# Kernel optimization log

Hardware: AMD Instinct MI355X
Metric: run time of the kernel (lower is better)

The kernel has to match this reference:

```python
import jax, jax.numpy as jnp
import numpy as np

SKIP = 2
EPS = 1e-9
K_PEN = 0.01
MU_BG = 0.0
VAR_BG = 100.0
SIZ = (256, 256, 256)
SIZA = (160, 192, 160)
NC = 10
COMPS = np.array([2, 2, 1, 1, 2, 1, 1, 2, 1])
NG = int(COMPS.sum())  # 13
FSIZ = (13, 13, 13)  # round(256*1.0/20)


def setup_inputs() -> dict:
    key = jax.random.key(0)
    ks = jax.random.split(key, 10)
    I = jax.random.uniform(ks[0], SIZ, jnp.float32)
    A = jax.random.uniform(ks[1], (*SIZA, NC), jnp.float32)
    A = A / jnp.sum(A, axis=-1, keepdims=True)  # probabilistic atlas
    aff_I = jnp.eye(4, dtype=jnp.float32)
    aff_A = jnp.diag(jnp.array([SIZ[0] / SIZA[0], SIZ[1] / SIZA[1], SIZ[2] / SIZA[2], 1.0], jnp.float32))
    mus = jax.random.uniform(ks[2], (NG,), jnp.float32)
    vars_ = 0.05 + 0.1 * jax.random.uniform(ks[3], (NG,), jnp.float32)
    w = np.asarray(jax.random.uniform(ks[4], (NG,))) + 0.1
    cls = np.repeat(np.arange(len(COMPS)), COMPS)
    onehot = (cls[:, None] == np.arange(len(COMPS))[None, :]).astype(np.float32)
    w = w / (onehot @ (onehot.T @ w))  # weights sum to 1 within each class
    weights = jnp.asarray(w, jnp.float32)
    gmm_onehot = jnp.asarray(onehot)
    ts = 0.5 * jax.random.normal(ks[5], (3,), jnp.float32)
    thetas = 2.0 * jax.random.normal(ks[6], (3,), jnp.float32)  # degrees
    scalings = 0.5 * jax.random.normal(ks[7], (3,), jnp.float32)
    shears = 0.5 * jax.random.normal(ks[8], (3,), jnp.float32)
    FIELD = 0.5 * jax.random.normal(ks[9], (*FSIZ, 3), jnp.float32)
    return dict(I=I, A=A, aff_I=aff_I, aff_A=aff_A, mus=mus, vars_=vars_, weights=weights,
                gmm_onehot=gmm_onehot, ts=ts, thetas=thetas, scalings=scalings,
                shears=shears, FIELD=FIELD)


def _bspline3(t):
    t = jnp.abs(t)
    return jnp.where(t < 1, (4.0 - 6.0 * t * t + 3.0 * t * t * t) / 6.0,
                     jnp.where(t < 2, (2.0 - t) ** 3 / 6.0, 0.0))


def _cubic_matrix(coords, n):
    # dense [m, n] cubic-B-spline sampling matrix with circular (dft) boundary,
    # prefilter=False (FIELD values treated as spline coefficients)
    m = coords.shape[0]
    base = jnp.floor(coords).astype(jnp.int32)
    W = jnp.zeros((m, n), coords.dtype)
    rows = jnp.arange(m)
    for k in (-1, 0, 1, 2):
        node = base + k
        W = W.at[rows, node % n].add(_bspline3(coords - node))
    return W


def reference(I, A, aff_I, aff_A, mus, vars_, weights, gmm_onehot, ts, thetas, scalings, shears, FIELD):
    nxA, nyA, nzA, C = A.shape
    fx, fy, fz = FIELD.shape[:3]
    dt = I.dtype

    # ---- affine from parameters (T @ Sh @ Sc @ Rz @ Ry @ Rx) ----
    th = thetas * (jnp.pi / 180.0)
    sh = shears / 100.0
    sc = jnp.exp(scalings / 20.0)
    c, s = jnp.cos(th), jnp.sin(th)
    Rx = jnp.array([[1.0, 0.0, 0.0, 0.0], [0.0, c[0], -s[0], 0.0], [0.0, s[0], c[0], 0.0], [0.0, 0.0, 0.0, 1.0]])
    Ry = jnp.array([[c[1], 0.0, s[1], 0.0], [0.0, 1.0, 0.0, 0.0], [-s[1], 0.0, c[1], 0.0], [0.0, 0.0, 0.0, 1.0]])
    Rz = jnp.array([[c[2], -s[2], 0.0, 0.0], [s[2], c[2], 0.0, 0.0], [0.0, 0.0, 1.0, 0.0], [0.0, 0.0, 0.0, 1.0]])
    Sc = jnp.diag(jnp.concatenate([sc, jnp.ones((1,), sc.dtype)]))
    Sh = jnp.array([[1.0, sh[1], sh[2], 0.0], [sh[0], 1.0, sh[2], 0.0], [sh[0], sh[1], 1.0, 0.0], [0.0, 0.0, 0.0, 1.0]])
    T = jnp.eye(4, dtype=dt).at[:3, 3].set(ts)
    AFF = T @ Sh @ Sc @ Rz @ Ry @ Rx
    V = jnp.linalg.inv(AFF @ aff_A) @ aff_I  # image voxel -> atlas voxel

    # ---- cubic-spline resample of deformation field (separable grid) ----
    xs = jnp.arange(0, I.shape[0], SKIP).astype(dt)
    ys = jnp.arange(0, I.shape[1], SKIP).astype(dt)
    zs = jnp.arange(0, I.shape[2], SKIP).astype(dt)
    field_f = FIELD / 100.0 * jnp.array([nxA, nyA, nzA], dt)  # [fx,fy,fz,3]
    Wx = _cubic_matrix(fx * xs / I.shape[0], fx)
    Wy = _cubic_matrix(fy * ys / I.shape[1], fy)
    Wz = _cubic_matrix(fz * zs / I.shape[2], fz)
    t1 = jnp.einsum('ia,abcd->ibcd', Wx, field_f)
    t1 = jnp.einsum('jb,ibcd->ijcd', Wy, t1)
    field_rs = jnp.einsum('kc,ijcd->ijkd', Wz, t1)  # [X,Y,Z,3]

    X = xs[:, None, None]
    Y = ys[None, :, None]
    Z = zs[None, None, :]
    gx = V[0, 0] * X + V[0, 1] * Y + V[0, 2] * Z + V[0, 3] + field_rs[..., 0]
    gy = V[1, 0] * X + V[1, 1] * Y + V[1, 2] * Z + V[1, 3] + field_rs[..., 1]
    gz = V[2, 0] * X + V[2, 1] * Y + V[2, 2] * Z + V[2, 3] + field_rs[..., 2]

    # ---- trilinear pull of atlas (zero bound, no extrapolation) ----
    x0 = jnp.floor(gx).astype(jnp.int32); rx = gx - x0
    y0 = jnp.floor(gy).astype(jnp.int32); ry = gy - y0
    z0 = jnp.floor(gz).astype(jnp.int32); rz = gz - z0
    Af = A.reshape(-1, C)
    acc = jnp.zeros((*gx.shape, C), dt)
    for dx in (0, 1):
        ix = x0 + dx; wx = rx if dx else 1.0 - rx
        vx = (ix >= 0) & (ix < nxA); ixc = jnp.clip(ix, 0, nxA - 1)
        for dy in (0, 1):
            iy = y0 + dy; wy = ry if dy else 1.0 - ry
            vy = (iy >= 0) & (iy < nyA); iyc = jnp.clip(iy, 0, nyA - 1)
            for dz in (0, 1):
                iz = z0 + dz; wz = rz if dz else 1.0 - rz
                vz = (iz >= 0) & (iz < nzA); izc = jnp.clip(iz, 0, nzA - 1)
                w = jnp.where(vx & vy & vz, wx * wy * wz, 0.0)
                flat = (ixc * nyA + iyc) * nzA + izc
                vals = jnp.take(Af, flat.reshape(-1), axis=0).reshape(*flat.shape, C)
                acc = acc + w[..., None] * vals

    atlas_rs = jnp.clip(acc, 0.0, 1.0)
    missing = 1.0 - jnp.sum(atlas_rs, axis=-1)
    prior_bg = jnp.clip(atlas_rs[..., 0] + missing, 0.0, 1.0)
    priors_rest = atlas_rs[..., 1:]  # already clipped to [0,1]
    priors = jnp.concatenate([prior_bg[..., None], priors_rest], axis=-1)

    # ---- GMM likelihoods ----
    Iskip = I[::SKIP, ::SKIP, ::SKIP]
    gl_bg = jnp.exp(-0.5 * (Iskip - MU_BG) ** 2 / VAR_BG) / jnp.sqrt(2.0 * jnp.pi * VAR_BG)
    gl = jnp.exp(-0.5 * (Iskip[..., None] - mus) ** 2 / vars_) / jnp.sqrt(2.0 * jnp.pi * vars_)  # [X,Y,Z,NG]
    class_lh = jnp.einsum('xyzg,gc->xyzc', weights * gl, gmm_onehot)  # per-class mixture
    normalizer = prior_bg * gl_bg + jnp.sum(priors_rest * class_lh, axis=-1)
    log_lh = jnp.log(EPS + normalizer)

    # ---- gradient penalty on field in voxel units of the full image grid ----
    siz_vec = jnp.array(I.shape, dt)
    fsiz_vec = jnp.array(FIELD.shape[:3], dt)
    fv = field_f * (fsiz_vec / siz_vec)
    pen = (jnp.mean((fv[1:] - fv[:-1]) ** 2)
           + jnp.mean((fv[:, 1:] - fv[:, :-1]) ** 2)
           + jnp.mean((fv[:, :, 1:] - fv[:, :, :-1]) ** 2)) / 3.0
    def_pen = K_PEN * pen
    loss = -jnp.mean(log_lh) + def_pen
    grids_new = jnp.stack([gx, gy, gz], axis=-1)
    return (loss, grids_new, priors, def_pen)
```

## Files before the change

kernel.cpp:

```cpp
#include <hip/hip_runtime.h>

#define PI_D 3.14159265358979323846
#define NS 128
#define NVOX (NS*NS*NS)
#define NBLK (NVOX/256)

typedef float f4v __attribute__((ext_vector_type(4)));
typedef f4v f4u __attribute__((aligned(8)));


static __device__ __forceinline__ float bspline3f(float t) {
    t = fabsf(t);
    if (t < 1.0f) return (4.0f - 6.0f*t*t + 3.0f*t*t*t) * (1.0f/6.0f);
    if (t < 2.0f) { float u = 2.0f - t; return u*u*u * (1.0f/6.0f); }
    return 0.0f;
}

static __device__ void mm4(const double* Am, const double* Bm, double* Cm) {
    for (int i = 0; i < 4; i++)
        for (int j = 0; j < 4; j++) {
            double s = 0.0;
            for (int k = 0; k < 4; k++) s += Am[i*4+k] * Bm[k*4+j];
            Cm[i*4+j] = s;
        }
}

static __device__ void inv4(const double* Am, double* Om) {
    double a[4][8];
    for (int i = 0; i < 4; i++)
        for (int j = 0; j < 4; j++) {
            a[i][j]   = Am[i*4+j];
            a[i][4+j] = (i == j) ? 1.0 : 0.0;
        }
    for (int col = 0; col < 4; col++) {
        int piv = col; double best = fabs(a[col][col]);
        for (int r = col+1; r < 4; r++) {
            double v = fabs(a[r][col]);
            if (v > best) { best = v; piv = r; }
        }
        if (piv != col)
            for (int j = 0; j < 8; j++) { double t = a[col][j]; a[col][j] = a[piv][j]; a[piv][j] = t; }
        double d = a[col][col];
        for (int j = 0; j < 8; j++) a[col][j] /= d;
        for (int r = 0; r < 4; r++) if (r != col) {
            double f = a[r][col];
            for (int j = 0; j < 8; j++) a[r][j] -= f * a[col][j];
        }
    }
    for (int i = 0; i < 4; i++)
        for (int j = 0; j < 4; j++) Om[i*4+j] = a[i][4+j];
}


__global__ void AD_prep(const float* __restrict__ aff_I, const float* __restrict__ aff_A,
                        const float* __restrict__ ts, const float* __restrict__ thetas,
                        const float* __restrict__ scalings, const float* __restrict__ shears,
                        const float* __restrict__ FIELD,
                        const float* __restrict__ vars_, const float* __restrict__ weights,
                        const float* __restrict__ mus,
                        float* __restrict__ wsf, int* __restrict__ wsi)
{
    const int tid = threadIdx.x;

    if (tid == 0) {
        double c0 = cos((double)thetas[0]*(PI_D/180.0)), s0 = sin((double)thetas[0]*(PI_D/180.0));
        double c1 = cos((double)thetas[1]*(PI_D/180.0)), s1 = sin((double)thetas[1]*(PI_D/180.0));
        double c2 = cos((double)thetas[2]*(PI_D/180.0)), s2 = sin((double)thetas[2]*(PI_D/180.0));
        double Rx[16] = {1,0,0,0,  0,c0,-s0,0,  0,s0,c0,0,  0,0,0,1};
        double Ry[16] = {c1,0,s1,0,  0,1,0,0,  -s1,0,c1,0,  0,0,0,1};
        double Rz[16] = {c2,-s2,0,0,  s2,c2,0,0,  0,0,1,0,  0,0,0,1};
        double t1[16], t2[16];
        mm4(Ry, Rx, t1);
        mm4(Rz, t1, t2);
        double sc0 = exp((double)scalings[0]/20.0);
        double sc1 = exp((double)scalings[1]/20.0);
        double sc2 = exp((double)scalings[2]/20.0);
        for (int j = 0; j < 4; j++) { t2[0*4+j] *= sc0; t2[1*4+j] *= sc1; t2[2*4+j] *= sc2; }
        double sh0 = (double)shears[0]/100.0, sh1 = (double)shears[1]/100.0, sh2 = (double)shears[2]/100.0;
        double Sh[16] = {1,sh1,sh2,0,  sh0,1,sh2,0,  sh0,sh1,1,0,  0,0,0,1};
        mm4(Sh, t2, t1);
        t1[3]  += (double)ts[0];
        t1[7]  += (double)ts[1];
        t1[11] += (double)ts[2];
        double Aa[16]; for (int i = 0; i < 16; i++) Aa[i] = (double)aff_A[i];
        mm4(t1, Aa, t2);
        double Mi[16]; inv4(t2, Mi);
        double Ai[16]; for (int i = 0; i < 16; i++) Ai[i] = (double)aff_I[i];
        mm4(Mi, Ai, t1);
        for (int i = 0; i < 16; i++) wsf[i] = (float)t1[i];
    }

    if (tid < 13) {
        float va = vars_[tid];
        wsf[17+tid] = weights[tid] / sqrtf(6.283185307179586f * va);
        wsf[32+tid] = -0.5f / va;
        wsf[48+tid] = mus[tid];
    }

    if (tid < 128) {
        for (int a = 0; a < 3; a++) {
            float coord = (13.0f * (float)(2*tid)) / 256.0f;
            int base = (int)floorf(coord);
            for (int k = 0; k < 4; k++) {
                int node = base + (k - 1);
                float w = bspline3f(coord - (float)node);
                int idx = node % 13; if (idx < 0) idx += 13;
                wsf[64 + (a*128+tid)*4 + k] = w;
                wsi[(a*128+tid)*4 + k] = idx;
            }
        }
    }

    __shared__ double red[256];
    double s = 0.0;
    for (int i = tid; i < 12*13*13*3; i += 256) {
        int d = i % 3; int r = i / 3; int cc = r % 13; r /= 13; int b = r % 13; int a = r / 13;
        float sf = (d == 1) ? 0.0975f : 0.08125f;
        float f1 = FIELD[(((a+1)*13+b)*13+cc)*3+d] * sf;
        float f0 = FIELD[(((a  )*13+b)*13+cc)*3+d] * sf;
        float df = f1 - f0; s += (double)(df*df);
    }
    for (int i = tid; i < 13*12*13*3; i += 256) {
        int d = i % 3; int r = i / 3; int cc = r % 13; r /= 13; int b = r % 12; int a = r / 12;
        float sf = (d == 1) ? 0.0975f : 0.08125f;
        float f1 = FIELD[((a*13+(b+1))*13+cc)*3+d] * sf;
        float f0 = FIELD[((a*13+(b  ))*13+cc)*3+d] * sf;
        float df = f1 - f0; s += (double)(df*df);
    }
    for (int i = tid; i < 13*13*12*3; i += 256) {
        int d = i % 3; int r = i / 3; int cc = r % 12; r /= 12; int b = r % 13; int a = r / 13;
        float sf = (d == 1) ? 0.0975f : 0.08125f;
        float f1 = FIELD[((a*13+b)*13+(cc+1))*3+d] * sf;
        float f0 = FIELD[((a*13+b)*13+(cc  ))*3+d] * sf;
        float df = f1 - f0; s += (double)(df*df);
    }
    red[tid] = s; __syncthreads();
    for (int st = 128; st > 0; st >>= 1) {
        if (tid < st) red[tid] += red[tid+st];
        __syncthreads();
    }
    if (tid == 0) wsf[16] = (float)(0.01 * red[0] / (6084.0 * 3.0));
}

__global__ void AD_field(const float* __restrict__ FIELD,
                         const float* __restrict__ wsf, const int* __restrict__ wsi,
                         float* __restrict__ tB)
{
    __shared__ float fld[13*13*13*3];
    const int tid = threadIdx.x;
    for (int i = tid; i < 13*13*13*3; i += 256) {
        int d = i - (i/3)*3;
        float sc = (d == 1) ? 1.92f : 1.6f;
        fld[i] = FIELD[i] * sc;
    }
    __syncthreads();

    const int p = blockIdx.x*256 + tid;
    const int j = p & 127, i = p >> 7;

    const float4 wx = *(const float4*)(wsf + 64 + (0*128+i)*4);
    const float4 wy = *(const float4*)(wsf + 64 + (1*128+j)*4);
    const int4  ix4 = *(const int4*)(wsi + (0*128+i)*4);
    const int4  iy4 = *(const int4*)(wsi + (1*128+j)*4);
    const float wxa[4] = {wx.x, wx.y, wx.z, wx.w};
    const float wya[4] = {wy.x, wy.y, wy.z, wy.w};
    const int   ixa[4] = {ix4.x, ix4.y, ix4.z, ix4.w};
    const int   iya[4] = {iy4.x, iy4.y, iy4.z, iy4.w};

    float acc[39];
    #pragma unroll
    for (int t = 0; t < 39; t++) acc[t] = 0.f;

    #pragma unroll
    for (int a = 0; a < 4; a++) {
        #pragma unroll
        for (int b = 0; b < 4; b++) {
            const float wab = wxa[a] * wya[b];
            const float* src = fld + (ixa[a]*13 + iya[b]) * 39;
            #pragma unroll
            for (int t = 0; t < 39; t++) acc[t] = fmaf(wab, src[t], acc[t]);
        }
    }
    float* dst = tB + (size_t)p * 39;
    #pragma unroll
    for (int t = 0; t < 39; t++) dst[t] = acc[t];
}

__launch_bounds__(256)
__global__ void AD_main(const float* __restrict__ I, const float* __restrict__ A,
                        const float* __restrict__ wsf, const int* __restrict__ wsi,
                        const float* __restrict__ tB,
                        double* __restrict__ partials, float* __restrict__ out)
{
    __shared__ float sh[80];
    __shared__ double wred[4];
    const int tid = threadIdx.x;

    {
        const float* src = tB + (size_t)(blockIdx.x * 2) * 39;
        if (tid < 78) sh[tid] = src[tid];
    }
    __syncthreads();

    const int v = blockIdx.x*256 + tid;
    const int z = v & 127, y = (v >> 7) & 127, x = v >> 14;

    const float4 wzv = *(const float4*)(wsf + 64 + (2*128+z)*4);
    const int4  izv = *(const int4*)(wsi + (2*128+z)*4);
    const float* myrow = sh + (tid >> 7) * 39;

    float fr0, fr1, fr2;
    {
        const float* r0 = myrow + izv.x*3;
        const float* r1 = myrow + izv.y*3;
        const float* r2 = myrow + izv.z*3;
        const float* r3 = myrow + izv.w*3;
        fr0 = wzv.x*r0[0] + wzv.y*r1[0] + wzv.z*r2[0] + wzv.w*r3[0];
        fr1 = wzv.x*r0[1] + wzv.y*r1[1] + wzv.z*r2[1] + wzv.w*r3[1];
        fr2 = wzv.x*r0[2] + wzv.y*r1[2] + wzv.z*r2[2] + wzv.w*r3[2];
    }

    const float X = (float)(2*x), Yf = (float)(2*y), Zf = (float)(2*z);
    const float gx = wsf[0]*X + wsf[1]*Yf + wsf[2]*Zf  + wsf[3]  + fr0;
    const float gy = wsf[4]*X + wsf[5]*Yf + wsf[6]*Zf  + wsf[7]  + fr1;
    const float gz = wsf[8]*X + wsf[9]*Yf + wsf[10]*Zf + wsf[11] + fr2;

    float* grids = out + 1;
    __builtin_nontemporal_store(gx, grids + (size_t)v*3 + 0);
    __builtin_nontemporal_store(gy, grids + (size_t)v*3 + 1);
    __builtin_nontemporal_store(gz, grids + (size_t)v*3 + 2);

    const float x0f = floorf(gx), y0f = floorf(gy), z0f = floorf(gz);
    const int x0 = (int)x0f, y0 = (int)y0f, z0 = (int)z0f;
    const float rx = gx - x0f, ry = gy - y0f, rz = gz - z0f;

    int lx[2], ly[2]; float wxt[2], wyt[2], wzt[2];
    lx[0] = x0   < 0 ? 0 : (x0   > 159 ? 159 : x0);
    lx[1] = x0+1 < 0 ? 0 : (x0+1 > 159 ? 159 : x0+1);
    ly[0] = y0   < 0 ? 0 : (y0   > 191 ? 191 : y0);
    ly[1] = y0+1 < 0 ? 0 : (y0+1 > 191 ? 191 : y0+1);
    wxt[0] = (x0   >= 0 && x0   < 160) ? (1.f - rx) : 0.f;
    wxt[1] = (x0+1 >= 0 && x0+1 < 160) ? rx : 0.f;
    wyt[0] = (y0   >= 0 && y0   < 192) ? (1.f - ry) : 0.f;
    wyt[1] = (y0+1 >= 0 && y0+1 < 192) ? ry : 0.f;
    wzt[0] = (z0   >= 0 && z0   < 160) ? (1.f - rz) : 0.f;
    wzt[1] = (z0+1 >= 0 && z0+1 < 160) ? rz : 0.f;

    const int zb = z0 < 0 ? 0 : (z0 > 158 ? 158 : z0);
    const bool hi0 = (z0 >= 159);
    const bool lo1 = (z0 < 0);

    float acc[10];
    #pragma unroll
    for (int c = 0; c < 10; c++) acc[c] = 0.f;

    #pragma unroll
    for (int ta = 0; ta < 2; ta++) {
        #pragma unroll
        for (int tb = 0; tb < 2; tb++) {
            const float wab = wxt[ta] * wyt[tb];
            const float w0 = wab * wzt[0];
            const float w1 = wab * wzt[1];
            const f4u* p = (const f4u*)(A + ((size_t)(lx[ta]*192 + ly[tb])*160 + zb)*10);
            const f4v L0 = p[0], L1 = p[1], L2 = p[2], L3 = p[3], L4 = p[4];
            const float lo[10] = {L0.x,L0.y,L0.z,L0.w, L1.x,L1.y,L1.z,L1.w, L2.x,L2.y};
            const float hiv[10] = {L2.z,L2.w, L3.x,L3.y,L3.z,L3.w, L4.x,L4.y,L4.z,L4.w};
            #pragma unroll
            for (int c = 0; c < 10; c++) {
                const float t0 = hi0 ? hiv[c] : lo[c];
                const float t1 = lo1 ? lo[c]  : hiv[c];
                acc[c] = fmaf(w0, t0, acc[c]);
                acc[c] = fmaf(w1, t1, acc[c]);
            }
        }
    }

    float pri[10]; float sum = 0.f;
    #pragma unroll
    for (int c = 0; c < 10; c++) {
        float t = acc[c]; t = t < 0.f ? 0.f : (t > 1.f ? 1.f : t);
        pri[c] = t; sum += t;
    }
    float p0 = pri[0] + (1.0f - sum);
    pri[0] = p0 < 0.f ? 0.f : (p0 > 1.f ? 1.f : p0);

    float* priors = out + 1 + (size_t)NVOX*3 + (size_t)v*10;
    #pragma unroll
    for (int c = 0; c < 10; c++) __builtin_nontemporal_store(pri[c], priors + c);

    const float Iv = __builtin_nontemporal_load(I + ((size_t)(2*x)*256 + (size_t)(2*y))*256 + (size_t)(2*z));
    const float gl_bg = expf(-0.005f*Iv*Iv) * 0.039894228040143274f;

    constexpr int CLS[13] = {0,0,1,1,2,3,4,4,5,6,7,7,8};
    float lh[9];
    #pragma unroll
    for (int c = 0; c < 9; c++) lh[c] = 0.f;
    #pragma unroll
    for (int g = 0; g < 13; g++) {
        const float dlt = Iv - wsf[48+g];
        lh[CLS[g]] += wsf[17+g] * expf(dlt*dlt*wsf[32+g]);
    }
    float nrm = pri[0] * gl_bg;
    #pragma unroll
    for (int c = 0; c < 9; c++) nrm = fmaf(pri[c+1], lh[c], nrm);
    const float ll = logf(1e-9f + nrm);

    double s = (double)ll;
    #pragma unroll
    for (int off = 32; off > 0; off >>= 1) s += __shfl_down(s, off, 64);
    if ((tid & 63) == 0) wred[tid >> 6] = s;
    __syncthreads();
    if (tid == 0) partials[blockIdx.x] = (wred[0] + wred[1]) + (wred[2] + wred[3]);
}

__global__ void AD_fin(const double* __restrict__ partials, const float* __restrict__ wsf,
                       float* __restrict__ out, int out_size)
{
    __shared__ double red[256];
    const int tid = threadIdx.x;
    double s = 0.0;
    for (int i = tid; i < NBLK; i += 256) s += partials[i];
    red[tid] = s; __syncthreads();
    for (int st = 128; st > 0; st >>= 1) {
        if (tid < st) red[tid] += red[tid+st];
        __syncthreads();
    }
    if (tid == 0) {
        float dp = wsf[16];
        out[0] = (float)(-(red[0] / (double)NVOX) + (double)dp);
        out[out_size-1] = dp;
    }
}

extern "C" void kernel_launch(void* const* d_in, const int* in_sizes, int n_in,
                              void* d_out, int out_size, void* d_ws, size_t ws_size,
                              hipStream_t stream)
{
    const float* I        = (const float*)d_in[0];
    const float* A        = (const float*)d_in[1];
    const float* aff_I    = (const float*)d_in[2];
    const float* aff_A    = (const float*)d_in[3];
    const float* mus      = (const float*)d_in[4];
    const float* vars_    = (const float*)d_in[5];
    const float* weights  = (const float*)d_in[6];
    const float* ts       = (const float*)d_in[8];
    const float* thetas   = (const float*)d_in[9];
    const float* scalings = (const float*)d_in[10];
    const float* shears   = (const float*)d_in[11];
    const float* FIELD    = (const float*)d_in[12];

    float* out = (float*)d_out;
    float* wsf = (float*)d_ws;
    int*   wsi = (int*)(wsf + 1600);
    double* partials = (double*)((char*)d_ws + 16384);
    float* tB = (float*)((char*)d_ws + 131072);

    hipLaunchKernelGGL(AD_prep, dim3(1), dim3(256), 0, stream,
                       aff_I, aff_A, ts, thetas, scalings, shears, FIELD, vars_, weights, mus, wsf, wsi);
    hipLaunchKernelGGL(AD_field, dim3(64), dim3(256), 0, stream,
                       FIELD, wsf, wsi, tB);
    hipLaunchKernelGGL(AD_main, dim3(NBLK), dim3(256), 0, stream,
                       I, A, wsf, wsi, tB, partials, out);
    hipLaunchKernelGGL(AD_fin, dim3(1), dim3(256), 0, stream,
                       partials, wsf, out, out_size);
}
```

Before: 129.0 us.

## Stage grid and prior outputs in LDS for coalesced vector stores; swizzle block order

Each thread used to write its 3 grid values and 10 priors straight to global memory with strided scalar stores. These outputs are now staged in shared memory and written back as contiguous 16-byte vector stores after the block's final barrier. Blocks are also remapped so that consecutive hardware blocks handle spread-out voxel ranges, likely to balance work or memory channels across XCDs. The change costs about 13 KB of extra LDS per block, which may lower occupancy, and the 4-byte-aligned vector type may not produce full-width stores.

```diff
diff --git a/kernel.cpp b/kernel.cpp
--- a/kernel.cpp
+++ b/kernel.cpp
@@ -7,6 +7,7 @@
 
 typedef float f4v __attribute__((ext_vector_type(4)));
 typedef f4v f4u __attribute__((aligned(8)));
+typedef float f4s __attribute__((ext_vector_type(4), aligned(4)));
 
 
 static __device__ __forceinline__ float bspline3f(float t) {
@@ -194,15 +195,19 @@
 {
     __shared__ float sh[80];
     __shared__ double wred[4];
+    __shared__ __align__(16) float sg[768];
+    __shared__ __align__(16) float sp[2560];
     const int tid = threadIdx.x;
 
+    const int wg = ((blockIdx.x & 7) << 10) + (blockIdx.x >> 3);
+
     {
-        const float* src = tB + (size_t)(blockIdx.x * 2) * 39;
+        const float* src = tB + (size_t)(wg * 2) * 39;
         if (tid < 78) sh[tid] = src[tid];
     }
     __syncthreads();
 
-    const int v = blockIdx.x*256 + tid;
+    const int v = wg*256 + tid;
     const int z = v & 127, y = (v >> 7) & 127, x = v >> 14;
 
     const float4 wzv = *(const float4*)(wsf + 64 + (2*128+z)*4);
@@ -225,10 +230,7 @@
     const float gy = wsf[4]*X + wsf[5]*Yf + wsf[6]*Zf  + wsf[7]  + fr1;
     const float gz = wsf[8]*X + wsf[9]*Yf + wsf[10]*Zf + wsf[11] + fr2;
 
-    float* grids = out + 1;
-    __builtin_nontemporal_store(gx, grids + (size_t)v*3 + 0);
-    __builtin_nontemporal_store(gy, grids + (size_t)v*3 + 1);
-    __builtin_nontemporal_store(gz, grids + (size_t)v*3 + 2);
+    sg[tid*3+0] = gx; sg[tid*3+1] = gy; sg[tid*3+2] = gz;
 
     const float x0f = floorf(gx), y0f = floorf(gy), z0f = floorf(gz);
     const int x0 = (int)x0f, y0 = (int)y0f, z0 = (int)z0f;
@@ -284,9 +286,8 @@
     float p0 = pri[0] + (1.0f - sum);
     pri[0] = p0 < 0.f ? 0.f : (p0 > 1.f ? 1.f : p0);
 
-    float* priors = out + 1 + (size_t)NVOX*3 + (size_t)v*10;
-    #pragma unroll
-    for (int c = 0; c < 10; c++) __builtin_nontemporal_store(pri[c], priors + c);
+    #pragma unroll
+    for (int c = 0; c < 10; c++) sp[tid*10+c] = pri[c];
 
     const float Iv = __builtin_nontemporal_load(I + ((size_t)(2*x)*256 + (size_t)(2*y))*256 + (size_t)(2*z));
     const float gl_bg = expf(-0.005f*Iv*Iv) * 0.039894228040143274f;
@@ -310,7 +311,21 @@
     for (int off = 32; off > 0; off >>= 1) s += __shfl_down(s, off, 64);
     if ((tid & 63) == 0) wred[tid >> 6] = s;
     __syncthreads();
-    if (tid == 0) partials[blockIdx.x] = (wred[0] + wred[1]) + (wred[2] + wred[3]);
+    if (tid == 0) partials[wg] = (wred[0] + wred[1]) + (wred[2] + wred[3]);
+
+    {
+        const f4s* g4 = (const f4s*)sg;
+        f4s* gdst = (f4s*)(out + 1) + (size_t)wg*192;
+        if (tid < 192) __builtin_nontemporal_store(g4[tid], gdst + tid);
+
+        const f4s* p4 = (const f4s*)sp;
+        f4s* pdst = (f4s*)(out + 1 + (size_t)NVOX*3) + (size_t)wg*640;
+        #pragma unroll
+        for (int k = 0; k < 3; k++) {
+            int j = k*256 + tid;
+            if (j < 640) __builtin_nontemporal_store(p4[j], pdst + j);
+        }
+    }
 }
 
 __global__ void AD_fin(const double* __restrict__ partials, const float* __restrict__ wsf,
```

After: 116.8 us, median of 2. -9.5%, faster.
